# Optimization experiments

Hardware: AMD Instinct MI355X
Metric: run time of the kernel (lower is better)

Reference implementation:

```python
import jax, jax.numpy as jnp
import numpy as np


def setup_inputs() -> dict:
    key = jax.random.key(0)
    k1, k2, k3 = jax.random.split(key, 3)
    B, C, H, W = 8, 128, 128, 128
    kh, kw = 5, 5
    x = jax.random.normal(k1, (B, C, H, W), dtype=jnp.float32)
    weight = jax.random.normal(k2, (B, C, kh, kw), dtype=jnp.float32)
    bias = jax.random.normal(k3, (B, C), dtype=jnp.float32)
    return {"x": x, "weight": weight, "bias": bias, "padding": 2, "stride": 1}


def reference(x, weight, bias, padding, stride):
    # Morphological dilation with external SE: out = max_k(x_patch + w_k) + bias.
    # torch unfold zero-pads, so padded zeros legitimately participate in the max-plus.
    B, C, H, W = x.shape
    kh, kw = weight.shape[-2:]
    ph = pw = int(padding)
    sh = sw = int(stride)
    H2 = (H + 2 * ph - kh) // sh + 1
    W2 = (W + 2 * pw - kw) // sw + 1
    xp = jnp.pad(x, ((0, 0), (0, 0), (ph, ph), (pw, pw)))
    y = None
    # Fixed small kh*kw loop; each iter is a vectorized shifted-window max-plus.
    for di in range(kh):
        for dj in range(kw):
            patch = xp[:, :, di:di + sh * H2:sh, dj:dj + sw * W2:sw]  # B,C,H2,W2
            val = patch + weight[:, :, di, dj][:, :, None, None]
            y = val if y is None else jnp.maximum(y, val)
    return y + bias[:, :, None, None]
```

## Files before the change

### kernel.cpp

```cpp
#include <hip/hip_runtime.h>


static constexpr int H = 128, W = 128, KH = 5, KW = 5, PAD = 2;
static constexpr int RSTRIP = 8;
static constexpr int RBAND  = 64;
static constexpr int BANDS  = H / RBAND;

#define MAX3(a, b, c) fmaxf(fmaxf((a), (b)), (c))

__global__ __launch_bounds__(256) void dilation_kernel(
    const float* __restrict__ x,
    const float* __restrict__ wgt,
    const float* __restrict__ bias,
    float* __restrict__ out)
{
    const int plane = blockIdx.x / BANDS;
    const int band  = blockIdx.x % BANDS;
    const int tid = threadIdx.x;
    const int cg  = tid & 31;
    const int rs  = tid >> 5;
    const int j0  = cg * 4;
    const int base = band * RBAND + rs * RSTRIP;

    const float* __restrict__ xp = x   + (size_t)plane * (H * W);
    float*       __restrict__ op = out + (size_t)plane * (H * W);
    const float* __restrict__ wp = wgt + plane * (KH * KW);

    const float bi = bias[plane];
    float wk[KH * KW];
#pragma unroll
    for (int i = 0; i < KH * KW; ++i) wk[i] = wp[i] + bi;

    const bool cgL = (cg > 0);
    const bool cgR = (cg < 31);
    const int colL = cgL ? (j0 - 2) : 0;
    const int colR = cgR ? (j0 + 4) : (W - 2);

    float win[KH][8];

#define LOAD_ROW(SLOT, ROW, ROK)                                              \
    do {                                                                      \
        const bool rok_ = (ROK);                                              \
        const int  rowc_ = rok_ ? (ROW) : 0;                                  \
        const float* rp_ = xp + rowc_ * W;                                    \
        const float2 L_ = *reinterpret_cast<const float2*>(rp_ + colL);       \
        const float4 M_ = *reinterpret_cast<const float4*>(rp_ + j0);         \
        const float2 R_ = *reinterpret_cast<const float2*>(rp_ + colR);       \
        win[SLOT][0] = (rok_ && cgL) ? L_.x : 0.0f;                           \
        win[SLOT][1] = (rok_ && cgL) ? L_.y : 0.0f;                           \
        win[SLOT][2] = rok_ ? M_.x : 0.0f;                                    \
        win[SLOT][3] = rok_ ? M_.y : 0.0f;                                    \
        win[SLOT][4] = rok_ ? M_.z : 0.0f;                                    \
        win[SLOT][5] = rok_ ? M_.w : 0.0f;                                    \
        win[SLOT][6] = (rok_ && cgR) ? R_.x : 0.0f;                           \
        win[SLOT][7] = (rok_ && cgR) ? R_.y : 0.0f;                           \
    } while (0)

#pragma unroll
    for (int t = 0; t < KH - 1; ++t) {
        const int row = base - PAD + t;
        LOAD_ROW(t, row, row >= 0);
    }

#pragma unroll
    for (int it = 0; it < RSTRIP; ++it) {
        const int i = base + it;

        {
            const int row = i + PAD;
            const int slot = (it + KH - 1) % KH;
            LOAD_ROW(slot, row < H ? row : (H - 1), row < H);
        }

        float res[4];
#pragma unroll
        for (int k = 0; k < 4; ++k) {
            float v[KH * KW];
#pragma unroll
            for (int r = 0; r < KH; ++r) {
                const int s = (it + r) % KH;
#pragma unroll
                for (int c = 0; c < KW; ++c)
                    v[r * KW + c] = win[s][k + c] + wk[r * KW + c];
            }
            const float u0 = MAX3(v[0],  v[1],  v[2]);
            const float u1 = MAX3(v[3],  v[4],  v[5]);
            const float u2 = MAX3(v[6],  v[7],  v[8]);
            const float u3 = MAX3(v[9],  v[10], v[11]);
            const float u4 = MAX3(v[12], v[13], v[14]);
            const float u5 = MAX3(v[15], v[16], v[17]);
            const float u6 = MAX3(v[18], v[19], v[20]);
            const float u7 = MAX3(v[21], v[22], v[23]);
            const float w0 = MAX3(u0, u1, u2);
            const float w1 = MAX3(u3, u4, u5);
            const float w2 = MAX3(u6, u7, v[24]);
            res[k] = MAX3(w0, w1, w2);
        }

        float4 o;
        o.x = res[0]; o.y = res[1]; o.z = res[2]; o.w = res[3];
        *reinterpret_cast<float4*>(op + i * W + j0) = o;
    }
#undef LOAD_ROW
}

extern "C" void kernel_launch(void* const* d_in, const int* in_sizes, int n_in,
                              void* d_out, int out_size, void* d_ws, size_t ws_size,
                              hipStream_t stream) {
    const float* x    = (const float*)d_in[0];
    const float* wgt  = (const float*)d_in[1];
    const float* bias = (const float*)d_in[2];
    float* out        = (float*)d_out;

    const int planes = in_sizes[2];
    dim3 grid(planes * BANDS);
    dim3 block(256);
    dilation_kernel<<<grid, block, 0, stream>>>(x, wgt, bias, out);
}
```

Measured before the change: 126.7 us.

## Stage padded input tile in LDS via global_load_lds and shrink bands

Each block now loads a zero-padded 36x132 tile of its plane into LDS with direct global-to-LDS loads, then reads windows from LDS instead of issuing overlapping global loads with boundary masks. Each block covers 32 rows instead of 64, with each thread doing 4 rows, so the grid is twice as large. The bias is added once after the max instead of being folded into every weight. This removes redundant global reads and branchy padding logic, at the cost of LDS usage, a barrier, halo reloads across smaller bands, and possible LDS bank conflicts from the 132-float row pitch.

```diff
diff --git a/kernel.cpp b/kernel.cpp
--- a/kernel.cpp
+++ b/kernel.cpp
@@ -2,11 +2,18 @@
 
 
 static constexpr int H = 128, W = 128, KH = 5, KW = 5, PAD = 2;
-static constexpr int RSTRIP = 8;
-static constexpr int RBAND  = 64;
-static constexpr int BANDS  = H / RBAND;
+static constexpr int QROWS = 32;
+static constexpr int PROWS = QROWS + KH - 1;
+static constexpr int PCOLS = W + 2 * PAD;
+static constexpr int NQ    = H / QROWS;
 
 #define MAX3(a, b, c) fmaxf(fmaxf((a), (b)), (c))
+
+__device__ inline void gload_lds4(const float* g, float* l) {
+    __builtin_amdgcn_global_load_lds(
+        (const __attribute__((address_space(1))) void*)g,
+        (__attribute__((address_space(3))) void*)l, 4, 0, 0);
+}
 
 __global__ __launch_bounds__(256) void dilation_kernel(
     const float* __restrict__ x,
@@ -14,63 +21,78 @@
     const float* __restrict__ bias,
     float* __restrict__ out)
 {
-    const int plane = blockIdx.x / BANDS;
-    const int band  = blockIdx.x % BANDS;
-    const int tid = threadIdx.x;
-    const int cg  = tid & 31;
-    const int rs  = tid >> 5;
-    const int j0  = cg * 4;
-    const int base = band * RBAND + rs * RSTRIP;
+    __shared__ float tile[PROWS * PCOLS];
+
+    const int plane = blockIdx.x / NQ;
+    const int q     = blockIdx.x % NQ;
+    const int tid   = threadIdx.x;
 
     const float* __restrict__ xp = x   + (size_t)plane * (H * W);
     float*       __restrict__ op = out + (size_t)plane * (H * W);
     const float* __restrict__ wp = wgt + plane * (KH * KW);
 
-    const float bi = bias[plane];
+    if (tid < 2 * PROWS) {
+        const int r   = tid >> 1;
+        const int off = (tid & 1) ? (PCOLS - 2) : 0;
+        tile[r * PCOLS + off]     = 0.0f;
+        tile[r * PCOLS + off + 1] = 0.0f;
+    }
+    if (q == 0 && tid < PCOLS) {
+        tile[tid]         = 0.0f;
+        tile[PCOLS + tid] = 0.0f;
+    }
+    if (q == NQ - 1 && tid < PCOLS) {
+        tile[(PROWS - 2) * PCOLS + tid] = 0.0f;
+        tile[(PROWS - 1) * PCOLS + tid] = 0.0f;
+    }
+
+    const int wave = tid >> 6;
+    const int lane = tid & 63;
+    const int row0 = q * QROWS - PAD;
+#pragma unroll
+    for (int chunk = 0; chunk < 2 * PROWS; chunk += 4) {
+        const int ch   = chunk + wave;
+        const int pr   = ch >> 1;
+        const int half = (ch & 1) * 64;
+        const int irow = row0 + pr;
+        if (irow >= 0 && irow < H) {
+            gload_lds4(xp + irow * W + half + lane,
+                       &tile[pr * PCOLS + PAD + half]);
+        }
+    }
+
+    __syncthreads();
+
     float wk[KH * KW];
 #pragma unroll
-    for (int i = 0; i < KH * KW; ++i) wk[i] = wp[i] + bi;
+    for (int i = 0; i < KH * KW; ++i) wk[i] = wp[i];
+    const float bi = bias[plane];
 
-    const bool cgL = (cg > 0);
-    const bool cgR = (cg < 31);
-    const int colL = cgL ? (j0 - 2) : 0;
-    const int colR = cgR ? (j0 + 4) : (W - 2);
+    const int cg = tid & 31;
+    const int rs = tid >> 5;
+    const int j0 = cg * 4;
+    const int tb = rs * 4;
 
     float win[KH][8];
 
-#define LOAD_ROW(SLOT, ROW, ROK)                                              \
+#define LOAD_TROW(SLOT, PR)                                                   \
     do {                                                                      \
-        const bool rok_ = (ROK);                                              \
-        const int  rowc_ = rok_ ? (ROW) : 0;                                  \
-        const float* rp_ = xp + rowc_ * W;                                    \
-        const float2 L_ = *reinterpret_cast<const float2*>(rp_ + colL);       \
-        const float4 M_ = *reinterpret_cast<const float4*>(rp_ + j0);         \
-        const float2 R_ = *reinterpret_cast<const float2*>(rp_ + colR);       \
-        win[SLOT][0] = (rok_ && cgL) ? L_.x : 0.0f;                           \
-        win[SLOT][1] = (rok_ && cgL) ? L_.y : 0.0f;                           \
-        win[SLOT][2] = rok_ ? M_.x : 0.0f;                                    \
-        win[SLOT][3] = rok_ ? M_.y : 0.0f;                                    \
-        win[SLOT][4] = rok_ ? M_.z : 0.0f;                                    \
-        win[SLOT][5] = rok_ ? M_.w : 0.0f;                                    \
-        win[SLOT][6] = (rok_ && cgR) ? R_.x : 0.0f;                           \
-        win[SLOT][7] = (rok_ && cgR) ? R_.y : 0.0f;                           \
+        const float* rp_ = &tile[(PR) * PCOLS + j0];                          \
+        const float4 a_ = *reinterpret_cast<const float4*>(rp_);              \
+        const float4 b_ = *reinterpret_cast<const float4*>(rp_ + 4);          \
+        win[SLOT][0] = a_.x; win[SLOT][1] = a_.y;                             \
+        win[SLOT][2] = a_.z; win[SLOT][3] = a_.w;                             \
+        win[SLOT][4] = b_.x; win[SLOT][5] = b_.y;                             \
+        win[SLOT][6] = b_.z; win[SLOT][7] = b_.w;                             \
     } while (0)
 
 #pragma unroll
-    for (int t = 0; t < KH - 1; ++t) {
-        const int row = base - PAD + t;
-        LOAD_ROW(t, row, row >= 0);
-    }
+    for (int t = 0; t < KH - 1; ++t)
+        LOAD_TROW(t, tb + t);
 
 #pragma unroll
-    for (int it = 0; it < RSTRIP; ++it) {
-        const int i = base + it;
-
-        {
-            const int row = i + PAD;
-            const int slot = (it + KH - 1) % KH;
-            LOAD_ROW(slot, row < H ? row : (H - 1), row < H);
-        }
+    for (int it = 0; it < 4; ++it) {
+        LOAD_TROW((it + KH - 1) % KH, tb + it + KH - 1);
 
         float res[4];
 #pragma unroll
@@ -94,14 +116,15 @@
             const float w0 = MAX3(u0, u1, u2);
             const float w1 = MAX3(u3, u4, u5);
             const float w2 = MAX3(u6, u7, v[24]);
-            res[k] = MAX3(w0, w1, w2);
+            res[k] = MAX3(w0, w1, w2) + bi;
         }
 
         float4 o;
         o.x = res[0]; o.y = res[1]; o.z = res[2]; o.w = res[3];
-        *reinterpret_cast<float4*>(op + i * W + j0) = o;
+        const int grow = q * QROWS + tb + it;
+        *reinterpret_cast<float4*>(op + grow * W + j0) = o;
     }
-#undef LOAD_ROW
+#undef LOAD_TROW
 }
 
 extern "C" void kernel_launch(void* const* d_in, const int* in_sizes, int n_in,
@@ -113,7 +136,7 @@
     float* out        = (float*)d_out;
 
     const int planes = in_sizes[2];
-    dim3 grid(planes * BANDS);
+    dim3 grid(planes * NQ);
     dim3 block(256);
     dilation_kernel<<<grid, block, 0, stream>>>(x, wgt, bias, out);
 }
```

Measured after the change: 122.5 us. 3.4% less time.
